# Kernel optimization log

Measured on AMD Instinct MI355X. Metric: run time of the kernel, lower is better.

Reference implementation:

```python
import jax, jax.numpy as jnp
import numpy as np

B, CIN, COUT, K, H, W, STYLE_DIM = 16, 128, 128, 3, 128, 128, 512

def setup_inputs() -> dict:
    key = jax.random.key(0)
    k1, k2, k3, k4 = jax.random.split(key, 4)
    x = jax.random.normal(k1, (B, CIN, H, W), dtype=jnp.float32)
    style = jax.random.normal(k2, (B, STYLE_DIM), dtype=jnp.float32)
    weight = jax.random.normal(k3, (COUT, CIN, K, K), dtype=jnp.float32)
    mod_w = jax.random.normal(k4, (CIN, STYLE_DIM), dtype=jnp.float32)
    mod_b = jnp.ones((CIN,), dtype=jnp.float32)  # EqualLinear bias_init=1
    return {"x": x, "style": style, "weight": weight, "mod_w": mod_w, "mod_b": mod_b}

def reference(x, style, weight, mod_w, mod_b):
    b, cin, h, w = x.shape
    cout, _, k, _ = weight.shape
    scale = 1.0 / np.sqrt(cin * k * k)        # conv equalized-lr scale
    lin_scale = 1.0 / np.sqrt(mod_w.shape[1])  # EqualLinear scale (lr_mul=1)
    pad = k // 2
    # affine modulation: EqualLinear(style_dim -> in_channels), bias_init=1
    s = style @ (mod_w * lin_scale).T + mod_b               # [B, Cin]
    # per-sample modulated weights
    wmod = scale * weight[None] * s[:, None, :, None, None]  # [B, Cout, Cin, k, k]
    demod = jax.lax.rsqrt(jnp.sum(wmod * wmod, axis=(2, 3, 4)) + 1e-8)  # [B, Cout]
    wmod = wmod * demod[:, :, None, None, None]
    # grouped conv with groups=batch == vmapped per-sample conv
    def conv_one(xi, wi):
        return jax.lax.conv_general_dilated(
            xi[None], wi, window_strides=(1, 1), padding=[(pad, pad), (pad, pad)],
            dimension_numbers=("NCHW", "OIHW", "NCHW"))[0]
    out = jax.vmap(conv_one)(x, wmod)  # [B, Cout, H, W]
    return out
```

## Files before the change

### kernel.cpp

```cpp
#include <hip/hip_runtime.h>
#include <hip/hip_bf16.h>


typedef __attribute__((ext_vector_type(8))) short short8;
typedef __attribute__((ext_vector_type(4))) float f32x4;

#define CONV_SCALE 0.029462782549439483f
#define LIN_SCALE 0.04419417382415922f

__device__ __forceinline__ void async16(unsigned short* lds, const unsigned short* g) {
  __builtin_amdgcn_global_load_lds((const __attribute__((address_space(1))) void*)g,
                                   (__attribute__((address_space(3))) void*)lds, 16, 0, 0);
}

__device__ __forceinline__ unsigned int pack2bf(float a, float b) {
  unsigned short ha = __builtin_bit_cast(unsigned short, __float2bfloat16(a));
  unsigned short hb = __builtin_bit_cast(unsigned short, __float2bfloat16(b));
  return (unsigned int)ha | ((unsigned int)hb << 16);
}

__global__ void style_kernel(const float* __restrict__ style, const float* __restrict__ mod_w,
                             const float* __restrict__ mod_b, float* __restrict__ s_ws) {
  const int gw = blockIdx.x * 4 + (threadIdx.x >> 6);
  const int b = gw >> 7, cin = gw & 127, lane = threadIdx.x & 63;
  const float4 s0 = *(const float4*)(style + (size_t)b * 512 + lane * 4);
  const float4 s1 = *(const float4*)(style + (size_t)b * 512 + 256 + lane * 4);
  const float4 w0 = *(const float4*)(mod_w + (size_t)cin * 512 + lane * 4);
  const float4 w1 = *(const float4*)(mod_w + (size_t)cin * 512 + 256 + lane * 4);
  float acc = s0.x * w0.x + s0.y * w0.y + s0.z * w0.z + s0.w * w0.w +
              s1.x * w1.x + s1.y * w1.y + s1.z * w1.z + s1.w * w1.w;
#pragma unroll
  for (int off = 32; off; off >>= 1) acc += __shfl_xor(acc, off);
  if (lane == 0) s_ws[b * 128 + cin] = acc * LIN_SCALE + mod_b[cin];
}

__global__ void modw_kernel(const float* __restrict__ weight, const float* __restrict__ s_ws,
                            unsigned short* __restrict__ w_ws) {
  const int bid = blockIdx.x;
  const int b = bid >> 7, cout = bid & 127;
  const int cin = threadIdx.x;
  const float sv = s_ws[b * 128 + cin] * CONV_SCALE;
  const float* wp = weight + ((size_t)cout * 128 + cin) * 9;
  float v[9];
  float ss = 0.f;
#pragma unroll
  for (int j = 0; j < 9; ++j) { v[j] = wp[j] * sv; ss += v[j] * v[j]; }
#pragma unroll
  for (int off = 32; off; off >>= 1) ss += __shfl_down(ss, off);
  __shared__ float red[2];
  if ((threadIdx.x & 63) == 0) red[threadIdx.x >> 6] = ss;
  __syncthreads();
  const float dem = rsqrtf(red[0] + red[1] + 1e-8f);
#pragma unroll
  for (int j = 0; j < 9; ++j) {
    __hip_bfloat16 h = __float2bfloat16(v[j] * dem);
    w_ws[(((size_t)b * 9 + j) * 128 + cout) * 128 + cin] =
        __builtin_bit_cast(unsigned short, h);
  }
}

__device__ __forceinline__ void transpose_row(const float* __restrict__ xb, int c0, int yy,
                                              unsigned short* __restrict__ dst, int tid) {
  const int tcq = tid & 15, txq = tid >> 4;
  if (yy < 0 || yy > 127) {
    const uint2 z = {0u, 0u};
#pragma unroll
    for (int i = 0; i < 4; ++i) {
      const int xp = txq * 4 + i;
      *(uint2*)(dst + xp * 64 + (((tcq >> 1) ^ (xp & 7)) << 3) + ((tcq & 1) << 2)) = z;
    }
    return;
  }
  const float* row = xb + (size_t)(c0 + tcq * 4) * 16384 + (size_t)yy * 128 + txq * 4;
  float4 f[4];
#pragma unroll
  for (int j = 0; j < 4; ++j) f[j] = *(const float4*)(row + (size_t)j * 16384);
#pragma unroll
  for (int i = 0; i < 4; ++i) {
    const int xp = txq * 4 + i;
    uint2 col;
    col.x = pack2bf(((const float*)&f[0])[i], ((const float*)&f[1])[i]);
    col.y = pack2bf(((const float*)&f[2])[i], ((const float*)&f[3])[i]);
    *(uint2*)(dst + xp * 64 + (((tcq >> 1) ^ (xp & 7)) << 3) + ((tcq & 1) << 2)) = col;
  }
}

__global__ __launch_bounds__(512, 2) void conv_kernel(const float* __restrict__ x,
                                                      const unsigned short* __restrict__ wws,
                                                      float* __restrict__ out) {
  __shared__ unsigned short xr[2 * 128 * 64];
  __shared__ unsigned short lA[128 * 64];

  const int tid = threadIdx.x;
  const int bid = (blockIdx.x & 7) * 128 + (blockIdx.x >> 3);
  const int b = bid >> 6, y0 = (bid & 63) * 2;
  const int lane = tid & 63, w = tid >> 6;
  const int wm = w & 1, wn = w >> 1;
  const int r = wn >> 1, xh = wn & 1;
  const int l15 = lane & 15, q = lane >> 4;

  f32x4 acc[4][4];
#pragma unroll
  for (int i = 0; i < 4; ++i)
#pragma unroll
    for (int t = 0; t < 4; ++t) acc[i][t] = (f32x4){0.f, 0.f, 0.f, 0.f};

  const float* xb = x + (size_t)b * (128 * 16384);
  const unsigned short* wb = wws + (size_t)b * 9 * 128 * 128;

  const int goff = (((tid & 7) ^ ((tid >> 3) & 7)) << 3);
  const int m0 = tid >> 3;
  const int eoff = tid * 8;

  int nt[4];
#pragma unroll
  for (int t = 0; t < 4; ++t) nt[t] = xh * 64 + t * 16 + l15;

  const short8 zero8 = {0, 0, 0, 0, 0, 0, 0, 0};

  for (int c0 = 0; c0 < 128; c0 += 64) {
    __syncthreads();
    transpose_row(xb, c0, y0 - 1, xr, tid);
    transpose_row(xb, c0, y0, xr + 8192, tid);
    for (int ky = 0; ky < 3; ++ky) {
      for (int kx = 0; kx < 3; ++kx) {
        const int j3 = ky * 3 + kx;
        if (j3) __syncthreads();
        async16(lA + eoff, wb + j3 * 16384 + c0 + m0 * 128 + goff);
        async16(lA + 4096 + eoff, wb + j3 * 16384 + c0 + (64 + m0) * 128 + goff);
        if (kx == 0 && ky > 0)
          transpose_row(xb, c0, y0 + ky, xr + (((ky + 1) & 1) << 13), tid);
        __syncthreads();
        const unsigned short* xkr = xr + (((ky + r) & 1) << 13);
        int xcb[4];
#pragma unroll
        for (int t = 0; t < 4; ++t) xcb[t] = nt[t] + (kx - 1);
        const bool lo = (xcb[0] < 0);
        const bool hi = (xcb[3] > 127);
        if (lo) xcb[0] = 0;
        if (hi) xcb[3] = 127;
#pragma unroll
        for (int s = 0; s < 2; ++s) {
          const int s4q = s * 4 + q;
          const int axor = ((s4q ^ (l15 & 7)) << 3);
          short8 af[4], bf[4];
#pragma unroll
          for (int i = 0; i < 4; ++i)
            af[i] = *(const short8*)(lA + (wm * 64 + i * 16 + l15) * 64 + axor);
#pragma unroll
          for (int t = 0; t < 4; ++t)
            bf[t] = *(const short8*)(xkr + xcb[t] * 64 + ((s4q ^ (xcb[t] & 7)) << 3));
          if (lo) bf[0] = zero8;
          if (hi) bf[3] = zero8;
#pragma unroll
          for (int i = 0; i < 4; ++i)
#pragma unroll
            for (int t = 0; t < 4; ++t)
              acc[i][t] = __builtin_amdgcn_mfma_f32_16x16x32_bf16(af[i], bf[t], acc[i][t], 0, 0, 0);
        }
      }
    }
  }

  float* ob = out + ((size_t)b * 128 * 128 + (y0 + r)) * 128;
#pragma unroll
  for (int i = 0; i < 4; ++i) {
    const int coutb = wm * 64 + i * 16 + q * 4;
#pragma unroll
    for (int rr = 0; rr < 4; ++rr) {
      float* orow = ob + (size_t)(coutb + rr) * (128 * 128);
#pragma unroll
      for (int t = 0; t < 4; ++t) orow[xh * 64 + t * 16 + l15] = acc[i][t][rr];
    }
  }
}

extern "C" void kernel_launch(void* const* d_in, const int* in_sizes, int n_in,
                              void* d_out, int out_size, void* d_ws, size_t ws_size,
                              hipStream_t stream) {
  const float* x = (const float*)d_in[0];
  const float* style = (const float*)d_in[1];
  const float* weight = (const float*)d_in[2];
  const float* mod_w = (const float*)d_in[3];
  const float* mod_b = (const float*)d_in[4];
  float* out = (float*)d_out;

  char* ws = (char*)d_ws;
  float* s_ws = (float*)ws;
  unsigned short* w_ws = (unsigned short*)(ws + 8192);

  style_kernel<<<512, 256, 0, stream>>>(style, mod_w, mod_b, s_ws);
  modw_kernel<<<16 * 128, 128, 0, stream>>>(weight, s_ws, w_ws);
  conv_kernel<<<16 * 64, 512, 0, stream>>>(x, w_ws, out);
}
```

Measured before the change: 316.8 us.

## Shrink conv blocks to one output row with 256 threads

Restructures the conv kernel so each 256-thread block computes a single output row instead of two, doubling the grid and raising the launch-bounds occupancy target to three blocks per CU. The input row transpose is adjusted so each thread handles two column chunks, and the ring of input rows is reduced to a simple two-buffer scheme. This aims for more waves and better latency hiding. In exchange, each weight tile and input row is reused across fewer output rows, so LDS fill and global traffic per output increase.

```diff
diff --git a/kernel.cpp b/kernel.cpp
--- a/kernel.cpp
+++ b/kernel.cpp
@@ -61,42 +61,47 @@
 
 __device__ __forceinline__ void transpose_row(const float* __restrict__ xb, int c0, int yy,
                                               unsigned short* __restrict__ dst, int tid) {
-  const int tcq = tid & 15, txq = tid >> 4;
+  const int tcq = tid & 15, t4 = tid >> 4;
   if (yy < 0 || yy > 127) {
     const uint2 z = {0u, 0u};
 #pragma unroll
+    for (int xi = 0; xi < 2; ++xi)
+#pragma unroll
+      for (int i = 0; i < 4; ++i) {
+        const int xp = (xi * 16 + t4) * 4 + i;
+        *(uint2*)(dst + xp * 64 + (((tcq >> 1) ^ (xp & 7)) << 3) + ((tcq & 1) << 2)) = z;
+      }
+    return;
+  }
+  const float* row = xb + (size_t)(c0 + tcq * 4) * 16384 + (size_t)yy * 128;
+#pragma unroll
+  for (int xi = 0; xi < 2; ++xi) {
+    const int xq = xi * 16 + t4;
+    float4 f[4];
+#pragma unroll
+    for (int j = 0; j < 4; ++j) f[j] = *(const float4*)(row + (size_t)j * 16384 + xq * 4);
+#pragma unroll
     for (int i = 0; i < 4; ++i) {
-      const int xp = txq * 4 + i;
-      *(uint2*)(dst + xp * 64 + (((tcq >> 1) ^ (xp & 7)) << 3) + ((tcq & 1) << 2)) = z;
+      const int xp = xq * 4 + i;
+      uint2 col;
+      col.x = pack2bf(((const float*)&f[0])[i], ((const float*)&f[1])[i]);
+      col.y = pack2bf(((const float*)&f[2])[i], ((const float*)&f[3])[i]);
+      *(uint2*)(dst + xp * 64 + (((tcq >> 1) ^ (xp & 7)) << 3) + ((tcq & 1) << 2)) = col;
     }
-    return;
-  }
-  const float* row = xb + (size_t)(c0 + tcq * 4) * 16384 + (size_t)yy * 128 + txq * 4;
-  float4 f[4];
-#pragma unroll
-  for (int j = 0; j < 4; ++j) f[j] = *(const float4*)(row + (size_t)j * 16384);
-#pragma unroll
-  for (int i = 0; i < 4; ++i) {
-    const int xp = txq * 4 + i;
-    uint2 col;
-    col.x = pack2bf(((const float*)&f[0])[i], ((const float*)&f[1])[i]);
-    col.y = pack2bf(((const float*)&f[2])[i], ((const float*)&f[3])[i]);
-    *(uint2*)(dst + xp * 64 + (((tcq >> 1) ^ (xp & 7)) << 3) + ((tcq & 1) << 2)) = col;
-  }
-}
-
-__global__ __launch_bounds__(512, 2) void conv_kernel(const float* __restrict__ x,
+  }
+}
+
+__global__ __launch_bounds__(256, 3) void conv_kernel(const float* __restrict__ x,
                                                       const unsigned short* __restrict__ wws,
                                                       float* __restrict__ out) {
   __shared__ unsigned short xr[2 * 128 * 64];
   __shared__ unsigned short lA[128 * 64];
 
   const int tid = threadIdx.x;
-  const int bid = (blockIdx.x & 7) * 128 + (blockIdx.x >> 3);
-  const int b = bid >> 6, y0 = (bid & 63) * 2;
+  const int bid = (blockIdx.x & 7) * 256 + (blockIdx.x >> 3);
+  const int b = bid >> 7, y = bid & 127;
   const int lane = tid & 63, w = tid >> 6;
   const int wm = w & 1, wn = w >> 1;
-  const int r = wn >> 1, xh = wn & 1;
   const int l15 = lane & 15, q = lane >> 4;
 
   f32x4 acc[4][4];
@@ -108,30 +113,30 @@
   const float* xb = x + (size_t)b * (128 * 16384);
   const unsigned short* wb = wws + (size_t)b * 9 * 128 * 128;
 
+  const int mbase = tid >> 3;
   const int goff = (((tid & 7) ^ ((tid >> 3) & 7)) << 3);
-  const int m0 = tid >> 3;
   const int eoff = tid * 8;
 
   int nt[4];
 #pragma unroll
-  for (int t = 0; t < 4; ++t) nt[t] = xh * 64 + t * 16 + l15;
+  for (int t = 0; t < 4; ++t) nt[t] = wn * 64 + t * 16 + l15;
 
   const short8 zero8 = {0, 0, 0, 0, 0, 0, 0, 0};
 
   for (int c0 = 0; c0 < 128; c0 += 64) {
     __syncthreads();
-    transpose_row(xb, c0, y0 - 1, xr, tid);
-    transpose_row(xb, c0, y0, xr + 8192, tid);
+    transpose_row(xb, c0, y - 1, xr, tid);
+    transpose_row(xb, c0, y, xr + 8192, tid);
     for (int ky = 0; ky < 3; ++ky) {
       for (int kx = 0; kx < 3; ++kx) {
         const int j3 = ky * 3 + kx;
         if (j3) __syncthreads();
-        async16(lA + eoff, wb + j3 * 16384 + c0 + m0 * 128 + goff);
-        async16(lA + 4096 + eoff, wb + j3 * 16384 + c0 + (64 + m0) * 128 + goff);
-        if (kx == 0 && ky > 0)
-          transpose_row(xb, c0, y0 + ky, xr + (((ky + 1) & 1) << 13), tid);
+#pragma unroll
+        for (int p = 0; p < 4; ++p)
+          async16(lA + p * 2048 + eoff, wb + j3 * 16384 + c0 + p * 4096 + mbase * 128 + goff);
+        if (ky == 1 && kx == 0) transpose_row(xb, c0, y + 1, xr, tid);
         __syncthreads();
-        const unsigned short* xkr = xr + (((ky + r) & 1) << 13);
+        const unsigned short* xkr = xr + ((ky & 1) << 13);
         int xcb[4];
 #pragma unroll
         for (int t = 0; t < 4; ++t) xcb[t] = nt[t] + (kx - 1);
@@ -162,7 +167,7 @@
     }
   }
 
-  float* ob = out + ((size_t)b * 128 * 128 + (y0 + r)) * 128;
+  float* ob = out + ((size_t)b * 128 * 128 + y) * 128;
 #pragma unroll
   for (int i = 0; i < 4; ++i) {
     const int coutb = wm * 64 + i * 16 + q * 4;
@@ -170,7 +175,7 @@
     for (int rr = 0; rr < 4; ++rr) {
       float* orow = ob + (size_t)(coutb + rr) * (128 * 128);
 #pragma unroll
-      for (int t = 0; t < 4; ++t) orow[xh * 64 + t * 16 + l15] = acc[i][t][rr];
+      for (int t = 0; t < 4; ++t) orow[wn * 64 + t * 16 + l15] = acc[i][t][rr];
     }
   }
 }
@@ -191,5 +196,5 @@
 
   style_kernel<<<512, 256, 0, stream>>>(style, mod_w, mod_b, s_ws);
   modw_kernel<<<16 * 128, 128, 0, stream>>>(weight, s_ws, w_ws);
-  conv_kernel<<<16 * 64, 512, 0, stream>>>(x, w_ws, out);
-}
+  conv_kernel<<<16 * 128, 256, 0, stream>>>(x, w_ws, out);
+}
```

Result: faster. 307.9 us (-2.8%).
